# Optimization experiments

Hardware: AMD Instinct MI355X
Metric: run time of the kernel (lower is better)

## Reference

```python
import jax, jax.numpy as jnp
import numpy as np

NUM_HEADS = 16
ROPE_BASE = 10000.0

def _rope(x):
    # x: (B, T, H, hd), rotate-half 1D RoPE over temporal axis
    B, T, H, hd = x.shape
    inv_freq = 1.0 / (ROPE_BASE ** (jnp.arange(0, hd, 2, dtype=jnp.float32) / hd))  # (hd/2,)
    freqs = jnp.arange(T, dtype=jnp.float32)[:, None] * inv_freq[None, :]            # (T, hd/2)
    emb = jnp.concatenate([freqs, freqs], axis=-1)                                    # (T, hd)
    cos = jnp.cos(emb)[None, :, None, :]
    sin = jnp.sin(emb)[None, :, None, :]
    x1, x2 = jnp.split(x, 2, axis=-1)
    rot = jnp.concatenate([-x2, x1], axis=-1)
    return x * cos + rot * sin

def setup_inputs() -> dict:
    key = jax.random.key(0)
    ks = jax.random.split(key, 7)
    B, T, S, D = 4, 16, 256, 2048
    std = 0.02
    return {
        'v_p': jax.random.normal(ks[0], (B, T, S, D), jnp.float32),
        'v_f': jax.random.normal(ks[1], (B, T, S, D), jnp.float32),
        'a_p': jax.random.normal(ks[2], (B, T, D), jnp.float32),
        'a_f': jax.random.normal(ks[3], (B, T, D), jnp.float32),
        'W_qkv': jax.random.normal(ks[4], (D, 3 * D), jnp.float32) * std,
        'W_proj': jax.random.normal(ks[5], (D, D), jnp.float32) * std,
        'b_proj': jnp.zeros((D,), jnp.float32),
    }

def reference(v_p, v_f, a_p, a_f, W_qkv, W_proj, b_proj):
    B, T_p, S, D = v_p.shape
    T_f = v_f.shape[1]
    H = NUM_HEADS
    hd = D // H
    scale = hd ** -0.5
    # pool spatial dim and concatenate streams: [v_p, v_f, a_p, a_f]
    tokens = jnp.concatenate([v_p.mean(axis=2), v_f.mean(axis=2), a_p, a_f], axis=1)  # (B, T, D)
    T = tokens.shape[1]
    qkv = tokens @ W_qkv  # qkv_bias=False
    q, k, v = jnp.split(qkv, 3, axis=-1)
    q = q.reshape(B, T, H, hd)
    k = k.reshape(B, T, H, hd)
    v = v.reshape(B, T, H, hd)
    q = _rope(q)
    k = _rope(k)
    scores = jnp.einsum('bqhd,bkhd->bhqk', q, k) * scale
    causal_mask = jnp.triu(jnp.ones((T, T), dtype=bool), k=1)
    scores = jnp.where(causal_mask[None, None], -jnp.inf, scores)
    attn = jax.nn.softmax(scores, axis=-1)
    out = jnp.einsum('bhqk,bkhd->bqhd', attn, v).reshape(B, T, D)
    out = out @ W_proj + b_proj
    v_p_out = jnp.broadcast_to(out[:, :T_p, None, :], (B, T_p, S, D))
    v_f_out = jnp.broadcast_to(out[:, T_p:T_p + T_f, None, :], (B, T_f, S, D))
    a_p_out = out[:, T_p + T_f:T_p + T_f + T_p]
    a_f_out = out[:, T_p + T_f + T_p:]
    return (v_p_out, v_f_out, a_p_out, a_f_out)
```

## Files before the change

### kernel.cpp

```cpp
#include <hip/hip_runtime.h>
#include <hip/hip_bf16.h>
#include <stdint.h>


using bf16x8v = __attribute__((ext_vector_type(8))) __bf16;
using f32x4v  = __attribute__((ext_vector_type(4))) float;

union Pack8 { __bf16 h[8]; uint4 u; };

__device__ __forceinline__ int swz(int r, int c) {
    return (r << 6) + ((c ^ (r & 7)) << 3);
}

__global__ __launch_bounds__(256) void prep_w_kernel(
    const float* __restrict__ W_qkv, const float* __restrict__ W_proj,
    __bf16* __restrict__ Wt_qkv, __bf16* __restrict__ Wt_proj)
{
    int bid = blockIdx.x;
    const float* src; __bf16* dst; int N, tile;
    if (bid < 3072) { src = W_qkv;  dst = Wt_qkv;  N = 6144; tile = bid; }
    else            { src = W_proj; dst = Wt_proj; N = 2048; tile = bid - 3072; }
    __shared__ float Ls[64][68];
    int tiles_n = N >> 6;
    int tn = tile % tiles_n;
    int tk = tile / tiles_n;
    int t = threadIdx.x;
    int rb = t >> 4;
    int c4 = (t & 15) << 2;
    #pragma unroll
    for (int s = 0; s < 4; ++s) {
        int r = rb + (s << 4);
        float4 v = *reinterpret_cast<const float4*>(
            src + (size_t)(tk * 64 + r) * N + tn * 64 + c4);
        *reinterpret_cast<float4*>(&Ls[r][c4]) = v;
    }
    __syncthreads();
    int c  = t >> 2;
    int r0 = (t & 3) << 4;
    Pack8 p0, p1;
    #pragma unroll
    for (int i = 0; i < 8; ++i) p0.h[i] = (__bf16)Ls[r0 + i][c];
    #pragma unroll
    for (int i = 0; i < 8; ++i) p1.h[i] = (__bf16)Ls[r0 + 8 + i][c];
    __bf16* drow = dst + (size_t)(tn * 64 + c) * 2048 + tk * 64 + r0;
    *reinterpret_cast<uint4*>(drow)     = p0.u;
    *reinterpret_cast<uint4*>(drow + 8) = p1.u;
}

__global__ __launch_bounds__(256) void mean_stage1_kernel(
    const float* __restrict__ v_p, const float* __restrict__ v_f,
    float* __restrict__ partials)
{
    int bid = blockIdx.x;
    int which  = bid >> 10;
    int rem    = bid & 1023;
    int row    = rem >> 4;
    int dchunk = (rem >> 3) & 1;
    int schunk = rem & 7;
    int d = (dchunk << 10) + (threadIdx.x << 2);
    const float* src = (which ? v_f : v_p) + ((size_t)row << 19)
                     + ((size_t)(schunk << 5) << 11) + d;
    float4 a = {0.f, 0.f, 0.f, 0.f};
    #pragma unroll 8
    for (int s = 0; s < 32; ++s) {
        float4 x = *reinterpret_cast<const float4*>(src + ((size_t)s << 11));
        a.x += x.x; a.y += x.y; a.z += x.z; a.w += x.w;
    }
    int pr = which * 64 + row;
    *reinterpret_cast<float4*>(&partials[(size_t)((pr << 3) + schunk) * 2048 + d]) = a;
}

__global__ __launch_bounds__(256) void tokens_finish_kernel(
    const float* __restrict__ partials, const float* __restrict__ a_p,
    const float* __restrict__ a_f, __bf16* __restrict__ tokens_bf)
{
    int bid = blockIdx.x;
    if (bid < 128) {
        int idx = (bid * 256 + threadIdx.x) * 8;
        int r = idx >> 11;
        int d = idx & 2047;
        float s[8];
        #pragma unroll
        for (int i = 0; i < 8; ++i) s[i] = 0.f;
        #pragma unroll
        for (int sc = 0; sc < 8; ++sc) {
            const float* p = partials + (size_t)((r << 3) + sc) * 2048 + d;
            float4 x0 = *reinterpret_cast<const float4*>(p);
            float4 x1 = *reinterpret_cast<const float4*>(p + 4);
            s[0] += x0.x; s[1] += x0.y; s[2] += x0.z; s[3] += x0.w;
            s[4] += x1.x; s[5] += x1.y; s[6] += x1.z; s[7] += x1.w;
        }
        const float inv = 1.f / 256.f;
        int which = r >> 6, rr = r & 63;
        int b = rr >> 4, tt = rr & 15;
        int tokrow = b * 64 + which * 16 + tt;
        Pack8 p;
        #pragma unroll
        for (int i = 0; i < 8; ++i) p.h[i] = (__bf16)(s[i] * inv);
        *reinterpret_cast<uint4*>(&tokens_bf[(size_t)tokrow * 2048 + d]) = p.u;
    } else {
        int g = (bid - 128) * 256 + threadIdx.x;
        int which = g >> 14;
        int j = g & 16383;
        int b = j >> 12;
        int rr = j & 4095;
        int tt = rr >> 8;
        int gq = rr & 255;
        const float* src = (which ? a_f : a_p) + (size_t)(b * 16 + tt) * 2048 + gq * 8;
        float4 x0 = *reinterpret_cast<const float4*>(src);
        float4 x1 = *reinterpret_cast<const float4*>(src + 4);
        Pack8 p;
        p.h[0] = (__bf16)x0.x; p.h[1] = (__bf16)x0.y; p.h[2] = (__bf16)x0.z; p.h[3] = (__bf16)x0.w;
        p.h[4] = (__bf16)x1.x; p.h[5] = (__bf16)x1.y; p.h[6] = (__bf16)x1.z; p.h[7] = (__bf16)x1.w;
        int tokrow = b * 64 + 32 + which * 16 + tt;
        *reinterpret_cast<uint4*>(&tokens_bf[(size_t)tokrow * 2048 + gq * 8]) = p.u;
    }
}

__global__ __launch_bounds__(256) void gemm_bf16_kernel(
    const __bf16* __restrict__ A, const __bf16* __restrict__ Bt,
    const float* __restrict__ bias, float* __restrict__ C, int N)
{
    __shared__ __bf16 As[4096];
    __shared__ __bf16 Bs[4096];
    const int t = threadIdx.x;
    const int m0 = blockIdx.y << 6;
    const int n0 = blockIdx.x << 6;
    const int lane = t & 63;
    const int w = t >> 6;
    const int wm = w << 4;
    const int lrow = lane & 15;
    const int lk = lane >> 4;
    const int srl = lane >> 3;
    const int schunk = lane & 7;

    f32x4v acc[4] = {{0.f,0.f,0.f,0.f},{0.f,0.f,0.f,0.f},
                     {0.f,0.f,0.f,0.f},{0.f,0.f,0.f,0.f}};

    int row_c0 = (w << 4) + srl;
    int row_c1 = row_c0 + 8;
    const __bf16* gA0 = A  + (size_t)(m0 + row_c0) * 2048 + ((schunk ^ (row_c0 & 7)) << 3);
    const __bf16* gA1 = A  + (size_t)(m0 + row_c1) * 2048 + ((schunk ^ (row_c1 & 7)) << 3);
    const __bf16* gB0 = Bt + (size_t)(n0 + row_c0) * 2048 + ((schunk ^ (row_c0 & 7)) << 3);
    const __bf16* gB1 = Bt + (size_t)(n0 + row_c1) * 2048 + ((schunk ^ (row_c1 & 7)) << 3);
    __bf16* lA0 = &As[(w << 4) << 6];
    __bf16* lA1 = &As[((w << 4) + 8) << 6];
    __bf16* lB0 = &Bs[(w << 4) << 6];
    __bf16* lB1 = &Bs[((w << 4) + 8) << 6];

    for (int kt = 0; kt < 32; ++kt) {
        __syncthreads();
        int ko = kt << 6;
        __builtin_amdgcn_global_load_lds(
            (const __attribute__((address_space(1))) void*)(gA0 + ko),
            (__attribute__((address_space(3))) void*)lA0, 16, 0, 0);
        __builtin_amdgcn_global_load_lds(
            (const __attribute__((address_space(1))) void*)(gA1 + ko),
            (__attribute__((address_space(3))) void*)lA1, 16, 0, 0);
        __builtin_amdgcn_global_load_lds(
            (const __attribute__((address_space(1))) void*)(gB0 + ko),
            (__attribute__((address_space(3))) void*)lB0, 16, 0, 0);
        __builtin_amdgcn_global_load_lds(
            (const __attribute__((address_space(1))) void*)(gB1 + ko),
            (__attribute__((address_space(3))) void*)lB1, 16, 0, 0);
        __syncthreads();
        #pragma unroll
        for (int s = 0; s < 2; ++s) {
            int cA = (s << 2) + lk;
            bf16x8v af = *reinterpret_cast<const bf16x8v*>(&As[swz(wm + lrow, cA)]);
            #pragma unroll
            for (int j = 0; j < 4; ++j) {
                bf16x8v bf = *reinterpret_cast<const bf16x8v*>(&Bs[swz((j << 4) + lrow, cA)]);
                acc[j] = __builtin_amdgcn_mfma_f32_16x16x32_bf16(af, bf, acc[j], 0, 0, 0);
            }
        }
    }
    #pragma unroll
    for (int j = 0; j < 4; ++j) {
        int col = n0 + (j << 4) + lrow;
        float bv = bias ? bias[col] : 0.f;
        #pragma unroll
        for (int e = 0; e < 4; ++e) {
            int row = m0 + wm + (lk << 2) + e;
            C[(size_t)row * N + col] = acc[j][e] + bv;
        }
    }
}

__global__ __launch_bounds__(256) void attn_kernel(
    const float* __restrict__ qkv, __bf16* __restrict__ attn_out)
{
    __shared__ float q_s[64 * 128];
    __shared__ float k_s[64 * 128];
    int b = blockIdx.x >> 4;
    int h = blockIdx.x & 15;
    int tid = threadIdx.x;
    const float* base = qkv + (size_t)(b * 64) * 6144 + h * 128;
    const float L2 = 0.20762050593046012f;
    #pragma unroll
    for (int r = 0; r < 4; ++r) {
        int idx = tid + (r << 8);
        int tq = idx >> 4;
        int d = (idx & 15) << 2;
        const float* srcr = base + (size_t)tq * 6144;
        float4 q1 = *reinterpret_cast<const float4*>(srcr + d);
        float4 q2 = *reinterpret_cast<const float4*>(srcr + d + 64);
        float4 k1 = *reinterpret_cast<const float4*>(srcr + 2048 + d);
        float4 k2 = *reinterpret_cast<const float4*>(srcr + 2048 + d + 64);
        float ft = (float)tq;
        float a0 = ft * exp2f(-(float)(d + 0) * L2);
        float a1 = ft * exp2f(-(float)(d + 1) * L2);
        float a2 = ft * exp2f(-(float)(d + 2) * L2);
        float a3 = ft * exp2f(-(float)(d + 3) * L2);
        float c0 = cosf(a0), s0 = sinf(a0);
        float c1 = cosf(a1), s1 = sinf(a1);
        float c2 = cosf(a2), s2 = sinf(a2);
        float c3 = cosf(a3), s3 = sinf(a3);
        float4 qa, qb, ka, kb;
        qa.x = q1.x * c0 - q2.x * s0;  qb.x = q2.x * c0 + q1.x * s0;
        qa.y = q1.y * c1 - q2.y * s1;  qb.y = q2.y * c1 + q1.y * s1;
        qa.z = q1.z * c2 - q2.z * s2;  qb.z = q2.z * c2 + q1.z * s2;
        qa.w = q1.w * c3 - q2.w * s3;  qb.w = q2.w * c3 + q1.w * s3;
        ka.x = k1.x * c0 - k2.x * s0;  kb.x = k2.x * c0 + k1.x * s0;
        ka.y = k1.y * c1 - k2.y * s1;  kb.y = k2.y * c1 + k1.y * s1;
        ka.z = k1.z * c2 - k2.z * s2;  kb.z = k2.z * c2 + k1.z * s2;
        ka.w = k1.w * c3 - k2.w * s3;  kb.w = k2.w * c3 + k1.w * s3;
        *reinterpret_cast<float4*>(&q_s[tq * 128 + d])      = qa;
        *reinterpret_cast<float4*>(&q_s[tq * 128 + d + 64]) = qb;
        *reinterpret_cast<float4*>(&k_s[tq * 128 + d])      = ka;
        *reinterpret_cast<float4*>(&k_s[tq * 128 + d + 64]) = kb;
    }
    __syncthreads();
    int qi = tid >> 2;
    int g  = tid & 3;
    float pv[16];
    #pragma unroll
    for (int j = 0; j < 16; ++j) pv[j] = 0.f;
    for (int d = 0; d < 128; d += 4) {
        float4 a = *reinterpret_cast<const float4*>(&q_s[qi * 128 + d]);
        #pragma unroll
        for (int j = 0; j < 16; ++j) {
            int ki = (j << 2) + g;
            float4 bb = *reinterpret_cast<const float4*>(&k_s[ki * 128 + d]);
            pv[j] += a.x * bb.x + a.y * bb.y + a.z * bb.z + a.w * bb.w;
        }
    }
    const float scale = 0.0883883476483184405f;
    float m = -1e30f;
    #pragma unroll
    for (int j = 0; j < 16; ++j) {
        int ki = (j << 2) + g;
        pv[j] = (ki <= qi) ? pv[j] * scale : -1e30f;
        m = fmaxf(m, pv[j]);
    }
    m = fmaxf(m, __shfl_xor(m, 1));
    m = fmaxf(m, __shfl_xor(m, 2));
    float l = 0.f;
    #pragma unroll
    for (int j = 0; j < 16; ++j) {
        float e = (pv[j] > -1e29f) ? expf(pv[j] - m) : 0.f;
        pv[j] = e;
        l += e;
    }
    l += __shfl_xor(l, 1);
    l += __shfl_xor(l, 2);
    float inv_l = 1.f / l;
    __syncthreads();
    float* p_s = q_s;
    #pragma unroll
    for (int j = 0; j < 16; ++j) p_s[qi * 65 + (j << 2) + g] = pv[j] * inv_l;
    float* v_s = k_s;
    #pragma unroll
    for (int r = 0; r < 8; ++r) {
        int idx = tid + (r << 8);
        int t = idx >> 5;
        int d = (idx & 31) << 2;
        *reinterpret_cast<float4*>(&v_s[t * 128 + d]) =
            *reinterpret_cast<const float4*>(base + (size_t)t * 6144 + 4096 + d);
    }
    __syncthreads();
    int d0 = g << 5;
    float4 acc[8];
    #pragma unroll
    for (int u = 0; u < 8; ++u) acc[u] = {0.f, 0.f, 0.f, 0.f};
    for (int ki = 0; ki < 64; ++ki) {
        float p = p_s[qi * 65 + ki];
        #pragma unroll
        for (int u = 0; u < 8; ++u) {
            float4 vv = *reinterpret_cast<const float4*>(&v_s[ki * 128 + d0 + (u << 2)]);
            acc[u].x += p * vv.x;
            acc[u].y += p * vv.y;
            acc[u].z += p * vv.z;
            acc[u].w += p * vv.w;
        }
    }
    __bf16* orow = attn_out + (size_t)(b * 64 + qi) * 2048 + h * 128 + d0;
    #pragma unroll
    for (int v = 0; v < 4; ++v) {
        Pack8 p;
        float4 a0 = acc[2 * v], a1 = acc[2 * v + 1];
        p.h[0] = (__bf16)a0.x; p.h[1] = (__bf16)a0.y; p.h[2] = (__bf16)a0.z; p.h[3] = (__bf16)a0.w;
        p.h[4] = (__bf16)a1.x; p.h[5] = (__bf16)a1.y; p.h[6] = (__bf16)a1.z; p.h[7] = (__bf16)a1.w;
        *reinterpret_cast<uint4*>(orow + v * 8) = p.u;
    }
}

__global__ __launch_bounds__(256) void outputs_kernel(
    const float* __restrict__ outp, float* __restrict__ d_out)
{
    int bid = blockIdx.x;
    if (bid < 2048) {
        int which = bid >> 10;
        int rem = bid & 1023;
        int row = rem >> 4;
        int schunk = rem & 15;
        int b = row >> 4;
        int t = row & 15;
        const float* src = outp + (size_t)(b * 64 + (which << 4) + t) * 2048 + threadIdx.x * 8;
        float4 o0 = *reinterpret_cast<const float4*>(src);
        float4 o1 = *reinterpret_cast<const float4*>(src + 4);
        size_t base = (size_t)which * 33554432 +
                      ((size_t)row * 256 + (size_t)schunk * 16) * 2048 + threadIdx.x * 8;
        float* dst = d_out + base;
        #pragma unroll
        for (int s = 0; s < 16; ++s) {
            *reinterpret_cast<float4*>(dst + (size_t)s * 2048)     = o0;
            *reinterpret_cast<float4*>(dst + (size_t)s * 2048 + 4) = o1;
        }
    } else {
        int g = (bid - 2048) * 256 + threadIdx.x;
        int which = g >> 14;
        int j = g & 16383;
        int b = j >> 12;
        int rr = j & 4095;
        int tt = rr >> 8;
        int gq = rr & 255;
        const float* src = outp + (size_t)(b * 64 + 32 + (which << 4) + tt) * 2048 + gq * 8;
        float4 x0 = *reinterpret_cast<const float4*>(src);
        float4 x1 = *reinterpret_cast<const float4*>(src + 4);
        float* dst = d_out + 67108864 + (size_t)which * 131072 +
                     (size_t)(b * 16 + tt) * 2048 + gq * 8;
        *reinterpret_cast<float4*>(dst)     = x0;
        *reinterpret_cast<float4*>(dst + 4) = x1;
    }
}

extern "C" void kernel_launch(void* const* d_in, const int* in_sizes, int n_in,
                              void* d_out, int out_size, void* d_ws, size_t ws_size,
                              hipStream_t stream)
{
    const float* v_p    = (const float*)d_in[0];
    const float* v_f    = (const float*)d_in[1];
    const float* a_p    = (const float*)d_in[2];
    const float* a_f    = (const float*)d_in[3];
    const float* W_qkv  = (const float*)d_in[4];
    const float* W_proj = (const float*)d_in[5];
    const float* b_proj = (const float*)d_in[6];
    float* out_f = (float*)d_out;

    char* ws = (char*)d_ws;
    __bf16* tokens_bf = (__bf16*)(ws);
    __bf16* Wt_qkv    = (__bf16*)(ws + 1048576);
    __bf16* Wt_proj   = (__bf16*)(ws + 26214400);
    float*  qkv       = (float*)(ws + 34603008);
    __bf16* attn_bf   = (__bf16*)(ws + 40894464);
    float*  outp      = (float*)(ws + 41943040);
    float*  partials  = (float*)(ws + 44040192);

    prep_w_kernel<<<4096, 256, 0, stream>>>(W_qkv, W_proj, Wt_qkv, Wt_proj);
    mean_stage1_kernel<<<2048, 256, 0, stream>>>(v_p, v_f, partials);
    tokens_finish_kernel<<<256, 256, 0, stream>>>(partials, a_p, a_f, tokens_bf);
    gemm_bf16_kernel<<<dim3(96, 4), 256, 0, stream>>>(tokens_bf, Wt_qkv, nullptr, qkv, 6144);
    attn_kernel<<<64, 256, 0, stream>>>(qkv, attn_bf);
    gemm_bf16_kernel<<<dim3(32, 4), 256, 0, stream>>>(attn_bf, Wt_proj, b_proj, outp, 2048);
    outputs_kernel<<<2176, 256, 0, stream>>>(outp, out_f);
}
```

Measured before the change: 241.1 us.

## Merge weight prep with spatial mean kernel and swizzle attention shared memory

Combines the weight transpose/convert kernel and the spatial-mean partial-sum kernel into one launch, with block ranges split between the two jobs. This removes a launch and lets the memory-bound mean reads overlap with the weight conversion. The attention kernel's Q/K/V shared-memory layout gets an XOR swizzle at float4 granularity to cut LDS bank conflicts, and the output store changes to interleaved 4-wide bf16 writes. The mean blocks now carry the weight path's shared-memory allocation, which may lower their occupancy.

```diff
diff --git a/kernel.cpp b/kernel.cpp
--- a/kernel.cpp
+++ b/kernel.cpp
@@ -7,67 +7,71 @@
 using f32x4v  = __attribute__((ext_vector_type(4))) float;
 
 union Pack8 { __bf16 h[8]; uint4 u; };
+union Pack4 { __bf16 h[4]; uint2 u; };
 
 __device__ __forceinline__ int swz(int r, int c) {
     return (r << 6) + ((c ^ (r & 7)) << 3);
 }
-
-__global__ __launch_bounds__(256) void prep_w_kernel(
+__device__ __forceinline__ int aswz(int r, int c) {
+    return (r << 7) + ((c ^ (r & 31)) << 2);
+}
+
+__global__ __launch_bounds__(256) void prep_mean_kernel(
+    const float* __restrict__ v_p, const float* __restrict__ v_f,
+    float* __restrict__ partials,
     const float* __restrict__ W_qkv, const float* __restrict__ W_proj,
     __bf16* __restrict__ Wt_qkv, __bf16* __restrict__ Wt_proj)
 {
-    int bid = blockIdx.x;
-    const float* src; __bf16* dst; int N, tile;
-    if (bid < 3072) { src = W_qkv;  dst = Wt_qkv;  N = 6144; tile = bid; }
-    else            { src = W_proj; dst = Wt_proj; N = 2048; tile = bid - 3072; }
     __shared__ float Ls[64][68];
-    int tiles_n = N >> 6;
-    int tn = tile % tiles_n;
-    int tk = tile / tiles_n;
-    int t = threadIdx.x;
-    int rb = t >> 4;
-    int c4 = (t & 15) << 2;
-    #pragma unroll
-    for (int s = 0; s < 4; ++s) {
-        int r = rb + (s << 4);
-        float4 v = *reinterpret_cast<const float4*>(
-            src + (size_t)(tk * 64 + r) * N + tn * 64 + c4);
-        *reinterpret_cast<float4*>(&Ls[r][c4]) = v;
-    }
-    __syncthreads();
-    int c  = t >> 2;
-    int r0 = (t & 3) << 4;
-    Pack8 p0, p1;
-    #pragma unroll
-    for (int i = 0; i < 8; ++i) p0.h[i] = (__bf16)Ls[r0 + i][c];
-    #pragma unroll
-    for (int i = 0; i < 8; ++i) p1.h[i] = (__bf16)Ls[r0 + 8 + i][c];
-    __bf16* drow = dst + (size_t)(tn * 64 + c) * 2048 + tk * 64 + r0;
-    *reinterpret_cast<uint4*>(drow)     = p0.u;
-    *reinterpret_cast<uint4*>(drow + 8) = p1.u;
-}
-
-__global__ __launch_bounds__(256) void mean_stage1_kernel(
-    const float* __restrict__ v_p, const float* __restrict__ v_f,
-    float* __restrict__ partials)
-{
-    int bid = blockIdx.x;
-    int which  = bid >> 10;
-    int rem    = bid & 1023;
-    int row    = rem >> 4;
-    int dchunk = (rem >> 3) & 1;
-    int schunk = rem & 7;
-    int d = (dchunk << 10) + (threadIdx.x << 2);
-    const float* src = (which ? v_f : v_p) + ((size_t)row << 19)
-                     + ((size_t)(schunk << 5) << 11) + d;
-    float4 a = {0.f, 0.f, 0.f, 0.f};
-    #pragma unroll 8
-    for (int s = 0; s < 32; ++s) {
-        float4 x = *reinterpret_cast<const float4*>(src + ((size_t)s << 11));
-        a.x += x.x; a.y += x.y; a.z += x.z; a.w += x.w;
-    }
-    int pr = which * 64 + row;
-    *reinterpret_cast<float4*>(&partials[(size_t)((pr << 3) + schunk) * 2048 + d]) = a;
+    int bid0 = blockIdx.x;
+    if (bid0 < 2048) {
+        int bid = bid0;
+        int which  = bid >> 10;
+        int rem    = bid & 1023;
+        int row    = rem >> 4;
+        int dchunk = (rem >> 3) & 1;
+        int schunk = rem & 7;
+        int d = (dchunk << 10) + (threadIdx.x << 2);
+        const float* src = (which ? v_f : v_p) + ((size_t)row << 19)
+                         + ((size_t)(schunk << 5) << 11) + d;
+        float4 a = {0.f, 0.f, 0.f, 0.f};
+        #pragma unroll 8
+        for (int s = 0; s < 32; ++s) {
+            float4 x = *reinterpret_cast<const float4*>(src + ((size_t)s << 11));
+            a.x += x.x; a.y += x.y; a.z += x.z; a.w += x.w;
+        }
+        int pr = which * 64 + row;
+        *reinterpret_cast<float4*>(&partials[(size_t)((pr << 3) + schunk) * 2048 + d]) = a;
+    } else {
+        int bid = bid0 - 2048;
+        const float* src; __bf16* dst; int N, tile;
+        if (bid < 3072) { src = W_qkv;  dst = Wt_qkv;  N = 6144; tile = bid; }
+        else            { src = W_proj; dst = Wt_proj; N = 2048; tile = bid - 3072; }
+        int tiles_n = N >> 6;
+        int tn = tile % tiles_n;
+        int tk = tile / tiles_n;
+        int t = threadIdx.x;
+        int rb = t >> 4;
+        int c4 = (t & 15) << 2;
+        #pragma unroll
+        for (int s = 0; s < 4; ++s) {
+            int r = rb + (s << 4);
+            float4 v = *reinterpret_cast<const float4*>(
+                src + (size_t)(tk * 64 + r) * N + tn * 64 + c4);
+            *reinterpret_cast<float4*>(&Ls[r][c4]) = v;
+        }
+        __syncthreads();
+        int c  = t >> 2;
+        int r0 = (t & 3) << 4;
+        Pack8 p0, p1;
+        #pragma unroll
+        for (int i = 0; i < 8; ++i) p0.h[i] = (__bf16)Ls[r0 + i][c];
+        #pragma unroll
+        for (int i = 0; i < 8; ++i) p1.h[i] = (__bf16)Ls[r0 + 8 + i][c];
+        __bf16* drow = dst + (size_t)(tn * 64 + c) * 2048 + tk * 64 + r0;
+        *reinterpret_cast<uint4*>(drow)     = p0.u;
+        *reinterpret_cast<uint4*>(drow + 8) = p1.u;
+    }
 }
 
 __global__ __launch_bounds__(256) void tokens_finish_kernel(
@@ -196,22 +200,23 @@
     int h = blockIdx.x & 15;
     int tid = threadIdx.x;
     const float* base = qkv + (size_t)(b * 64) * 6144 + h * 128;
-    const float L2 = 0.20762050593046012f;
+    const float L2C = 0.20762050593046012f;
     #pragma unroll
     for (int r = 0; r < 4; ++r) {
         int idx = tid + (r << 8);
         int tq = idx >> 4;
-        int d = (idx & 15) << 2;
+        int cg = idx & 15;
+        int d = cg << 2;
         const float* srcr = base + (size_t)tq * 6144;
         float4 q1 = *reinterpret_cast<const float4*>(srcr + d);
         float4 q2 = *reinterpret_cast<const float4*>(srcr + d + 64);
         float4 k1 = *reinterpret_cast<const float4*>(srcr + 2048 + d);
         float4 k2 = *reinterpret_cast<const float4*>(srcr + 2048 + d + 64);
         float ft = (float)tq;
-        float a0 = ft * exp2f(-(float)(d + 0) * L2);
-        float a1 = ft * exp2f(-(float)(d + 1) * L2);
-        float a2 = ft * exp2f(-(float)(d + 2) * L2);
-        float a3 = ft * exp2f(-(float)(d + 3) * L2);
+        float a0 = ft * exp2f(-(float)(d + 0) * L2C);
+        float a1 = ft * exp2f(-(float)(d + 1) * L2C);
+        float a2 = ft * exp2f(-(float)(d + 2) * L2C);
+        float a3 = ft * exp2f(-(float)(d + 3) * L2C);
         float c0 = cosf(a0), s0 = sinf(a0);
         float c1 = cosf(a1), s1 = sinf(a1);
         float c2 = cosf(a2), s2 = sinf(a2);
@@ -225,10 +230,10 @@
         ka.y = k1.y * c1 - k2.y * s1;  kb.y = k2.y * c1 + k1.y * s1;
         ka.z = k1.z * c2 - k2.z * s2;  kb.z = k2.z * c2 + k1.z * s2;
         ka.w = k1.w * c3 - k2.w * s3;  kb.w = k2.w * c3 + k1.w * s3;
-        *reinterpret_cast<float4*>(&q_s[tq * 128 + d])      = qa;
-        *reinterpret_cast<float4*>(&q_s[tq * 128 + d + 64]) = qb;
-        *reinterpret_cast<float4*>(&k_s[tq * 128 + d])      = ka;
-        *reinterpret_cast<float4*>(&k_s[tq * 128 + d + 64]) = kb;
+        *reinterpret_cast<float4*>(&q_s[aswz(tq, cg)])      = qa;
+        *reinterpret_cast<float4*>(&q_s[aswz(tq, cg + 16)]) = qb;
+        *reinterpret_cast<float4*>(&k_s[aswz(tq, cg)])      = ka;
+        *reinterpret_cast<float4*>(&k_s[aswz(tq, cg + 16)]) = kb;
     }
     __syncthreads();
     int qi = tid >> 2;
@@ -236,12 +241,12 @@
     float pv[16];
     #pragma unroll
     for (int j = 0; j < 16; ++j) pv[j] = 0.f;
-    for (int d = 0; d < 128; d += 4) {
-        float4 a = *reinterpret_cast<const float4*>(&q_s[qi * 128 + d]);
+    for (int c = 0; c < 32; ++c) {
+        float4 a = *reinterpret_cast<const float4*>(&q_s[aswz(qi, c)]);
         #pragma unroll
         for (int j = 0; j < 16; ++j) {
             int ki = (j << 2) + g;
-            float4 bb = *reinterpret_cast<const float4*>(&k_s[ki * 128 + d]);
+            float4 bb = *reinterpret_cast<const float4*>(&k_s[aswz(ki, c)]);
             pv[j] += a.x * bb.x + a.y * bb.y + a.z * bb.z + a.w * bb.w;
         }
     }
@@ -273,13 +278,12 @@
     #pragma unroll
     for (int r = 0; r < 8; ++r) {
         int idx = tid + (r << 8);
-        int t = idx >> 5;
-        int d = (idx & 31) << 2;
-        *reinterpret_cast<float4*>(&v_s[t * 128 + d]) =
-            *reinterpret_cast<const float4*>(base + (size_t)t * 6144 + 4096 + d);
+        int tv = idx >> 5;
+        int c = idx & 31;
+        *reinterpret_cast<float4*>(&v_s[aswz(tv, c)]) =
+            *reinterpret_cast<const float4*>(base + (size_t)tv * 6144 + 4096 + (c << 2));
     }
     __syncthreads();
-    int d0 = g << 5;
     float4 acc[8];
     #pragma unroll
     for (int u = 0; u < 8; ++u) acc[u] = {0.f, 0.f, 0.f, 0.f};
@@ -287,21 +291,20 @@
         float p = p_s[qi * 65 + ki];
         #pragma unroll
         for (int u = 0; u < 8; ++u) {
-            float4 vv = *reinterpret_cast<const float4*>(&v_s[ki * 128 + d0 + (u << 2)]);
+            float4 vv = *reinterpret_cast<const float4*>(&v_s[aswz(ki, g + (u << 2))]);
             acc[u].x += p * vv.x;
             acc[u].y += p * vv.y;
             acc[u].z += p * vv.z;
             acc[u].w += p * vv.w;
         }
     }
-    __bf16* orow = attn_out + (size_t)(b * 64 + qi) * 2048 + h * 128 + d0;
-    #pragma unroll
-    for (int v = 0; v < 4; ++v) {
-        Pack8 p;
-        float4 a0 = acc[2 * v], a1 = acc[2 * v + 1];
-        p.h[0] = (__bf16)a0.x; p.h[1] = (__bf16)a0.y; p.h[2] = (__bf16)a0.z; p.h[3] = (__bf16)a0.w;
-        p.h[4] = (__bf16)a1.x; p.h[5] = (__bf16)a1.y; p.h[6] = (__bf16)a1.z; p.h[7] = (__bf16)a1.w;
-        *reinterpret_cast<uint4*>(orow + v * 8) = p.u;
+    __bf16* orow = attn_out + (size_t)(b * 64 + qi) * 2048 + h * 128 + (g << 2);
+    #pragma unroll
+    for (int u = 0; u < 8; ++u) {
+        Pack4 p4;
+        p4.h[0] = (__bf16)acc[u].x; p4.h[1] = (__bf16)acc[u].y;
+        p4.h[2] = (__bf16)acc[u].z; p4.h[3] = (__bf16)acc[u].w;
+        *reinterpret_cast<uint2*>(orow + (u << 4)) = p4.u;
     }
 }
 
@@ -328,9 +331,9 @@
             *reinterpret_cast<float4*>(dst + (size_t)s * 2048 + 4) = o1;
         }
     } else {
-        int g = (bid - 2048) * 256 + threadIdx.x;
-        int which = g >> 14;
-        int j = g & 16383;
+        int g8 = (bid - 2048) * 256 + threadIdx.x;
+        int which = g8 >> 14;
+        int j = g8 & 16383;
         int b = j >> 12;
         int rr = j & 4095;
         int tt = rr >> 8;
@@ -367,8 +370,8 @@
     float*  outp      = (float*)(ws + 41943040);
     float*  partials  = (float*)(ws + 44040192);
 
-    prep_w_kernel<<<4096, 256, 0, stream>>>(W_qkv, W_proj, Wt_qkv, Wt_proj);
-    mean_stage1_kernel<<<2048, 256, 0, stream>>>(v_p, v_f, partials);
+    prep_mean_kernel<<<6144, 256, 0, stream>>>(v_p, v_f, partials,
+                                               W_qkv, W_proj, Wt_qkv, Wt_proj);
     tokens_finish_kernel<<<256, 256, 0, stream>>>(partials, a_p, a_f, tokens_bf);
     gemm_bf16_kernel<<<dim3(96, 4), 256, 0, stream>>>(tokens_bf, Wt_qkv, nullptr, qkv, 6144);
     attn_kernel<<<64, 256, 0, stream>>>(qkv, attn_bf);
```

New measurement: 218.7 us. 1.1x faster.
